# Kernel tuning notes

Measured on AMD Instinct MI355X. Metric: run time of the kernel, lower is better.

The kernel has to match this reference:

```python
import math
import jax, jax.numpy as jnp
import numpy as np

B, T = 2, 2048
D_MODEL, D_HEAD = 2048, 128
N_Q, N_KV = 16, 4
QPG = N_Q // N_KV  # queries per kv group
ROPE_BASE = 10000.0
YARN_SCALE = 4.0
ORIG_MAX_LEN = 4096
BETA_FAST, BETA_SLOW = 32.0, 1.0
RMS_EPS = 1.1920929e-07  # torch.finfo(float32).eps (nn.RMSNorm default)


def _yarn_inv_freq():
    inv = 1.0 / ROPE_BASE ** (np.arange(0, D_HEAD, 2, dtype=np.float32) / D_HEAD)
    wavelengths = 2.0 * math.pi / inv
    low_wavelen = ORIG_MAX_LEN / BETA_SLOW
    high_wavelen = ORIG_MAX_LEN / BETA_FAST
    gamma = np.clip((low_wavelen - wavelengths) / (low_wavelen - high_wavelen), 0.0, 1.0)
    return (gamma * inv + (1.0 - gamma) * inv / YARN_SCALE).astype(np.float32)

INV_FREQ = jnp.asarray(_yarn_inv_freq())  # (D_HEAD//2,) constant buffer
MSCALE = 0.1 * math.log(YARN_SCALE) + 1.0
ATTN_SCALE = 1.0 / (MSCALE * math.sqrt(D_HEAD))


def _rms_norm(x, w):
    # normalize over last dim (d_head), learnable per-dim weight
    return x * jax.lax.rsqrt(jnp.mean(x * x, axis=-1, keepdims=True) + RMS_EPS) * w


def _apply_rope(x):
    # x: (..., T, d_head)
    t = jnp.arange(x.shape[-2], dtype=jnp.float32)
    freqs = jnp.outer(t, INV_FREQ)                 # (T, d/2)
    emb = jnp.concatenate([freqs, freqs], axis=-1)  # (T, d)
    cos, sin = jnp.cos(emb), jnp.sin(emb)
    half = x.shape[-1] // 2
    x_rot = jnp.concatenate([-x[..., half:], x[..., :half]], axis=-1)
    return x * cos + x_rot * sin


def setup_inputs() -> dict:
    key = jax.random.key(0)
    ks = jax.random.split(key, 5)
    x = jax.random.normal(ks[0], (B, T, D_MODEL), dtype=jnp.float32)
    w_scale = 0.02
    Wq = jax.random.normal(ks[1], (D_MODEL, N_Q * D_HEAD), dtype=jnp.float32) * w_scale
    Wkv = jax.random.normal(ks[2], (D_MODEL, 2 * N_KV * D_HEAD), dtype=jnp.float32) * w_scale
    Wo = jax.random.normal(ks[3], (N_Q * D_HEAD, D_MODEL), dtype=jnp.float32) * w_scale
    q_norm_w = jnp.ones((D_HEAD,), dtype=jnp.float32)
    k_norm_w = jnp.ones((D_HEAD,), dtype=jnp.float32)
    return {"x": x, "Wq": Wq, "Wkv": Wkv, "Wo": Wo,
            "q_norm_w": q_norm_w, "k_norm_w": k_norm_w}


def reference(x, Wq, Wkv, Wo, q_norm_w, k_norm_w):
    b, t, _ = x.shape
    # projections
    q = (x @ Wq).reshape(b, t, QPG, N_KV, D_HEAD).transpose(0, 2, 3, 1, 4)  # (b,qpg,g,t,d)
    kv = x @ Wkv
    k, v = jnp.split(kv, 2, axis=-1)
    k = k.reshape(b, t, N_KV, D_HEAD).transpose(0, 2, 1, 3)  # (b,g,t,d)
    v = v.reshape(b, t, N_KV, D_HEAD).transpose(0, 2, 1, 3)  # (b,g,t,d)
    # RMSNorm + YaRN RoPE on q,k (math done in float32 as in source)
    q = _apply_rope(_rms_norm(q, q_norm_w))
    k = _apply_rope(_rms_norm(k, k_norm_w))
    # GQA replication: head index h = qpg*N_KV + g (matches source rearrange/reshape)
    q = q.reshape(b, N_Q, t, D_HEAD)
    k = jnp.broadcast_to(k[:, None], (b, QPG, N_KV, t, D_HEAD)).reshape(b, N_Q, t, D_HEAD)
    v = jnp.broadcast_to(v[:, None], (b, QPG, N_KV, t, D_HEAD)).reshape(b, N_Q, t, D_HEAD)
    # causal SDPA with custom scale
    scores = jnp.einsum('bhtd,bhsd->bhts', q, k) * ATTN_SCALE
    causal = jnp.tril(jnp.ones((t, t), dtype=bool))
    scores = jnp.where(causal, scores, jnp.finfo(scores.dtype).min)
    probs = jax.nn.softmax(scores, axis=-1)
    attn = jnp.einsum('bhts,bhsd->bhtd', probs, v)
    out = attn.transpose(0, 2, 1, 3).reshape(b, t, N_Q * D_HEAD)
    return out @ Wo
```

## Files before the change

kernel.cpp:

```cpp
#include <hip/hip_runtime.h>
#include <cmath>

typedef float f32x4 __attribute__((ext_vector_type(4)));
typedef __bf16 bf16x8 __attribute__((ext_vector_type(8)));

#define DEV static __device__ __forceinline__

DEV unsigned short f2bf(float f) {
  unsigned int u = __builtin_bit_cast(unsigned int, f);
  u += 0x7FFFu + ((u >> 16) & 1u);
  return (unsigned short)(u >> 16);
}
DEV float bf2f(unsigned short h) {
  unsigned int u = ((unsigned int)h) << 16;
  return __builtin_bit_cast(float, u);
}
DEV unsigned int cvtpk(float lo, float hi) {
  unsigned int r;
  asm("v_cvt_pk_bf16_f32 %0, %1, %2" : "=v"(r) : "v"(lo), "v"(hi));
  return r;
}
DEV f32x4 mfma16(bf16x8 a, bf16x8 b, f32x4 c) {
  return __builtin_amdgcn_mfma_f32_16x16x32_bf16(a, b, c, 0, 0, 0);
}
DEV void dma16(const void* g, void* l) {
  __builtin_amdgcn_global_load_lds(
      (const __attribute__((address_space(1))) void*)(uintptr_t)g,
      (__attribute__((address_space(3))) void*)(unsigned int)(uintptr_t)l,
      16, 0, 0);
}

constexpr int T_SEQ = 2048;

__global__ __launch_bounds__(256) void build_rope(float2* __restrict__ rope) {
  int gid = blockIdx.x * 256 + threadIdx.x;
  if (gid >= T_SEQ * 64) return;
  int t = gid >> 6, i = gid & 63;
  double inv = pow(10000.0, -((double)(2 * i)) / 128.0);
  double wl = 6.283185307179586 / inv;
  double gm = (4096.0 - wl) / (4096.0 - 128.0);
  gm = gm < 0.0 ? 0.0 : (gm > 1.0 ? 1.0 : gm);
  float f = (float)(gm * inv + (1.0 - gm) * inv * 0.25);
  float th = (float)t * f;
  float s, c;
  sincosf(th, &s, &c);
  rope[gid] = make_float2(c, s);
}

__global__ __launch_bounds__(256) void cvt_f32_bf16(const float4* __restrict__ in,
                                                    ushort* __restrict__ out, int n4) {
  int i = blockIdx.x * 256 + threadIdx.x;
  if (i >= n4) return;
  float4 v = in[i];
  unsigned int lo = (unsigned int)f2bf(v.x) | ((unsigned int)f2bf(v.y) << 16);
  unsigned int hi = (unsigned int)f2bf(v.z) | ((unsigned int)f2bf(v.w) << 16);
  int row = i >> 9;
  int e = (i * 4) & 2047;
  size_t o = ((size_t)row << 11) + (size_t)(e ^ ((row & 7) << 3));
  *(uint2*)(out + o) = make_uint2(lo, hi);
}

__global__ __launch_bounds__(256) void tconv(const float* __restrict__ in,
                                             ushort* __restrict__ out, int R, int C) {
  __shared__ ushort tile[64][65];
  int c0 = blockIdx.x * 64, r0 = blockIdx.y * 64;
  int j = threadIdx.x & 63, i0 = threadIdx.x >> 6;
#pragma unroll
  for (int ii = 0; ii < 16; ++ii) {
    int i = i0 + ii * 4;
    tile[i][j] = f2bf(in[(size_t)(r0 + i) * C + c0 + j]);
  }
  __syncthreads();
#pragma unroll
  for (int ii = 0; ii < 16; ++ii) {
    int jr = i0 + ii * 4;
    out[(size_t)(c0 + jr) * R + ((r0 + j) ^ ((jr & 7) << 3))] = tile[j][jr];
  }
}

template <int BM, int OUT_BF16>
__global__ __launch_bounds__(512) void gemm256(const ushort* __restrict__ A,
                                               const ushort* __restrict__ Bt,
                                               void* __restrict__ Cv,
                                               int M, int N, int K) {
  constexpr int MT = BM / 32;
  constexpr int NPH = MT / 2;
  constexpr int ADMA = BM / 64;
  __shared__ ushort lA[2][BM * 64];
  __shared__ ushort lB[2][256 * 64];
  const int tid = threadIdx.x, lane = tid & 63, w = tid >> 6;
  const int wm = (w >> 2) * (BM / 2);
  const int wn = (w & 3) * 64;
  const int m0 = blockIdx.y * BM, n0 = blockIdx.x * 256;

  f32x4 acc[MT][4] = {};

  const size_t K2 = (size_t)K * 2;
  const char* Ab = (const char*)A + (size_t)m0 * K2;
  const char* Bb = (const char*)Bt + (size_t)n0 * K2;
  const int srb = lane >> 3;
  const int scb = (lane & 7) * 16;

  auto stage = [&](int t, int bi) {
#pragma unroll
    for (int ii = 0; ii < ADMA; ++ii) {
      const int ar = w * (BM / 8) + ii * 8;
      dma16(Ab + (size_t)(ar + srb) * K2 + (size_t)t * 128 + scb,
            (char*)lA[bi] + ar * 128);
    }
#pragma unroll
    for (int ii = 0; ii < 4; ++ii) {
      const int br = w * 32 + ii * 8;
      dma16(Bb + (size_t)(br + srb) * K2 + (size_t)t * 128 + scb,
            (char*)lB[bi] + br * 128);
    }
  };

  stage(0, 0);
  const int nkt = K >> 6;

  for (int t = 0; t < nkt; ++t) {
    const int cur = t & 1;
    if (t + 1 < nkt) {
      stage(t + 1, cur ^ 1);
      if constexpr (BM == 256)
        asm volatile("s_waitcnt vmcnt(8)" ::: "memory");
      else
        asm volatile("s_waitcnt vmcnt(6)" ::: "memory");
    } else {
      asm volatile("s_waitcnt vmcnt(0)" ::: "memory");
    }
    __builtin_amdgcn_s_barrier();
    __builtin_amdgcn_sched_barrier(0);

    const char* lAc = (const char*)lA[cur];
    const char* lBc = (const char*)lB[cur];

#pragma unroll
    for (int ph = 0; ph < NPH; ++ph) {
      const int mb = (BM == 256) ? (ph >> 1) * 4 : 0;
      const int nb = (BM == 256) ? (ph & 1) * 2 : ph * 2;
#pragma unroll
      for (int kk = 0; kk < 2; ++kk) {
        bf16x8 af[4], bfr[2];
        const int byo = kk * 64 + ((lane >> 4) << 4);
#pragma unroll
        for (int i = 0; i < 4; ++i) {
          int row = wm + (mb + i) * 16 + (lane & 15);
          af[i] = *(const bf16x8*)(lAc + row * 128 + (byo ^ ((row & 7) << 4)));
        }
#pragma unroll
        for (int i = 0; i < 2; ++i) {
          int row = wn + (nb + i) * 16 + (lane & 15);
          bfr[i] = *(const bf16x8*)(lBc + row * 128 + (byo ^ ((row & 7) << 4)));
        }
        __builtin_amdgcn_s_setprio(1);
#pragma unroll
        for (int i = 0; i < 4; ++i)
#pragma unroll
          for (int j = 0; j < 2; ++j)
            acc[mb + i][nb + j] = mfma16(af[i], bfr[j], acc[mb + i][nb + j]);
        __builtin_amdgcn_s_setprio(0);
      }
    }
    __builtin_amdgcn_sched_barrier(0);
    __builtin_amdgcn_s_barrier();
  }

  const int rr = (lane >> 4) << 2;
  const int cc = lane & 15;
  if (OUT_BF16) {
    ushort* C = (ushort*)Cv;
#pragma unroll
    for (int mt = 0; mt < MT; ++mt)
#pragma unroll
      for (int nt = 0; nt < 4; ++nt)
#pragma unroll
        for (int j = 0; j < 4; ++j) {
          int r = m0 + wm + mt * 16 + rr + j;
          int c = n0 + wn + nt * 16 + cc;
          C[(size_t)r * N + c] = f2bf(acc[mt][nt][j]);
        }
  } else {
    float* C = (float*)Cv;
#pragma unroll
    for (int mt = 0; mt < MT; ++mt)
#pragma unroll
      for (int nt = 0; nt < 4; ++nt)
#pragma unroll
        for (int j = 0; j < 4; ++j) {
          int r = m0 + wm + mt * 16 + rr + j;
          int c = n0 + wn + nt * 16 + cc;
          C[(size_t)r * N + c] = acc[mt][nt][j];
        }
  }
}

__global__ __launch_bounds__(256) void norm_rope(const ushort* __restrict__ qkv,
                                                 const float* __restrict__ qw,
                                                 const float* __restrict__ kw,
                                                 const float2* __restrict__ rope,
                                                 ushort* __restrict__ qout,
                                                 ushort* __restrict__ kout,
                                                 float q_scale) {
  const int w = threadIdx.x >> 6, lane = threadIdx.x & 63;
  const int vi = blockIdx.x * 4 + w;
  const ushort* src;
  const float* wt;
  ushort* dst;
  float extra;
  int t, bb;
  if (vi < 65536) {
    int row = vi >> 4, H = vi & 15;
    bb = row >> 11;
    t = row & 2047;
    src = qkv + (size_t)row * 3072 + H * 128 + lane * 2;
    wt = qw;
    extra = q_scale;
    dst = qout + ((size_t)(bb * 16 + H) * T_SEQ + t) * 128 + lane * 2;
  } else {
    int vi2 = vi - 65536;
    int row = vi2 >> 2, gg = vi2 & 3;
    bb = row >> 11;
    t = row & 2047;
    src = qkv + (size_t)row * 3072 + 2048 + gg * 128 + lane * 2;
    wt = kw;
    extra = 1.f;
    dst = kout + ((size_t)(bb * 4 + gg) * T_SEQ + t) * 128 +
          ((lane * 2) ^ ((t & 7) << 3));
  }
  float x0 = bf2f(src[0]), x1 = bf2f(src[1]);
  float ss = x0 * x0 + x1 * x1;
#pragma unroll
  for (int d = 1; d < 64; d <<= 1) ss += __shfl_xor(ss, d, 64);
  float sc = rsqrtf(ss * (1.f / 128.f) + 1.1920929e-7f);
  float w0 = wt[lane * 2], w1 = wt[lane * 2 + 1];
  float xn0 = x0 * sc * w0, xn1 = x1 * sc * w1;
  float p0 = __shfl_xor(xn0, 32, 64), p1 = __shfl_xor(xn1, 32, 64);
  float r0 = lane < 32 ? -p0 : p0;
  float r1 = lane < 32 ? -p1 : p1;
  int i0 = (lane * 2) & 63;
  float2 cs0 = rope[t * 64 + i0];
  float2 cs1 = rope[t * 64 + i0 + 1];
  float o0 = (xn0 * cs0.x + r0 * cs0.y) * extra;
  float o1 = (xn1 * cs1.x + r1 * cs1.y) * extra;
  unsigned int pk = (unsigned int)f2bf(o0) | ((unsigned int)f2bf(o1) << 16);
  *(unsigned int*)dst = pk;
}

__global__ __launch_bounds__(256) void tv_kernel(const ushort* __restrict__ qkv,
                                                 ushort* __restrict__ vt) {
  __shared__ ushort tile[64][65];
  int t0 = blockIdx.x * 64;
  int y = blockIdx.y;
  int dh = y & 1, bg = y >> 1;
  int bb = bg >> 2, g = bg & 3;
  int j = threadIdx.x & 63, i0 = threadIdx.x >> 6;
#pragma unroll
  for (int ii = 0; ii < 16; ++ii) {
    int i = i0 + ii * 4;
    tile[i][j] = qkv[(size_t)(bb * T_SEQ + t0 + i) * 3072 + 2560 + g * 128 + dh * 64 + j];
  }
  __syncthreads();
#pragma unroll
  for (int ii = 0; ii < 16; ++ii) {
    int jr = i0 + ii * 4;
    vt[((size_t)bg * 128 + dh * 64 + jr) * T_SEQ + ((t0 + j) ^ ((jr & 7) << 3))] = tile[j][jr];
  }
}

__global__ __launch_bounds__(256, 2) void attn_fwd(const ushort* __restrict__ qh,
                                                   const ushort* __restrict__ kh,
                                                   const ushort* __restrict__ vt,
                                                   ushort* __restrict__ o) {
  const int f = blockIdx.x;
  const int half = f >> 8, c = f & 255;
  const int kk = c >> 5, bh = c & 31;
  const int qt = half ? kk : (15 - kk);
  const int b = bh >> 4, H = bh & 15;
  const int g = H & 3;
  const int tid = threadIdx.x, lane = tid & 63, w = tid >> 6;
  const int wrow0 = qt * 128 + w * 32;

  __shared__ ushort lK[2][64 * 128];
  __shared__ ushort lV[2][128 * 64];
  __shared__ ushort lP[4 * 32 * 64];

  bf16x8 qf[2][4];
#pragma unroll
  for (int mt = 0; mt < 2; ++mt) {
    const ushort* qb = qh + ((size_t)(b * 16 + H) * T_SEQ + wrow0 + mt * 16 + (lane & 15)) * 128 +
                       ((lane >> 4) << 3);
#pragma unroll
    for (int kc = 0; kc < 4; ++kc) qf[mt][kc] = *(const bf16x8*)(qb + kc * 32);
  }

  f32x4 oacc[2][8] = {};
  float mrow[2] = {-INFINITY, -INFINITY};
  float lrow[2] = {0.f, 0.f};

  const char* kpl = (const char*)(kh + (size_t)(b * 4 + g) * T_SEQ * 128);
  const char* vpl = (const char*)(vt + (size_t)(b * 4 + g) * 128 * T_SEQ);

  auto stage = [&](int j, int bi) {
#pragma unroll
    for (int ii = 0; ii < 4; ++ii) {
      const int off = w * 4096 + ii * 1024;
      dma16(kpl + (size_t)j * 16384 + off + lane * 16, (char*)lK[bi] + off);
      const int vrow = w * 32 + ii * 8 + (lane >> 3);
      dma16(vpl + (size_t)vrow * (T_SEQ * 2) + j * 128 + (lane & 7) * 16,
            (char*)lV[bi] + off);
    }
  };

  stage(0, 0);

  const int rsel = ((lane >> 4) << 2);

  const int jmax = 2 * qt + 1;
  for (int j = 0; j <= jmax; ++j) {
    const int cur = j & 1;
    if (j < jmax) {
      stage(j + 1, cur ^ 1);
      asm volatile("s_waitcnt vmcnt(8)" ::: "memory");
    } else {
      asm volatile("s_waitcnt vmcnt(0)" ::: "memory");
    }
    __builtin_amdgcn_s_barrier();
    __builtin_amdgcn_sched_barrier(0);

    f32x4 s[2][4];
#pragma unroll
    for (int nt = 0; nt < 4; ++nt) {
      bf16x8 kf[4];
      int krow = nt * 16 + (lane & 15);
#pragma unroll
      for (int kc = 0; kc < 4; ++kc) {
        int byo = kc * 64 + ((lane >> 4) << 4);
        kf[kc] = *(const bf16x8*)((const char*)lK[cur] + krow * 256 + (byo ^ ((krow & 7) << 4)));
      }
#pragma unroll
      for (int mt = 0; mt < 2; ++mt) {
        f32x4 a = {0.f, 0.f, 0.f, 0.f};
#pragma unroll
        for (int kc = 0; kc < 4; ++kc) a = mfma16(kf[kc], qf[mt][kc], a);
        s[mt][nt] = a;
      }
    }

    if (j * 64 + 63 > wrow0) {
#pragma unroll
      for (int mt = 0; mt < 2; ++mt) {
        int qrow = wrow0 + mt * 16 + (lane & 15);
#pragma unroll
        for (int nt = 0; nt < 4; ++nt)
#pragma unroll
          for (int jj = 0; jj < 4; ++jj) {
            int col = j * 64 + nt * 16 + rsel + jj;
            if (col > qrow) s[mt][nt][jj] = -3.0e38f;
          }
      }
    }

    float pm[2], mn[2];
#pragma unroll
    for (int mt = 0; mt < 2; ++mt) {
      float a0 = fmaxf(fmaxf(s[mt][0][0], s[mt][0][1]), fmaxf(s[mt][0][2], s[mt][0][3]));
      float a1 = fmaxf(fmaxf(s[mt][1][0], s[mt][1][1]), fmaxf(s[mt][1][2], s[mt][1][3]));
      float a2 = fmaxf(fmaxf(s[mt][2][0], s[mt][2][1]), fmaxf(s[mt][2][2], s[mt][2][3]));
      float a3 = fmaxf(fmaxf(s[mt][3][0], s[mt][3][1]), fmaxf(s[mt][3][2], s[mt][3][3]));
      float p = fmaxf(fmaxf(a0, a1), fmaxf(a2, a3));
      p = fmaxf(p, __shfl_xor(p, 16, 64));
      p = fmaxf(p, __shfl_xor(p, 32, 64));
      pm[mt] = p;
      mn[mt] = mrow[mt];
    }

    bool ok = (pm[0] <= mrow[0] + 11.5417f) && (pm[1] <= mrow[1] + 11.5417f);
    if (!__all(ok)) {
#pragma unroll
      for (int mt = 0; mt < 2; ++mt) {
        mn[mt] = fmaxf(mrow[mt], pm[mt]);
        float rsc = exp2f(mrow[mt] - mn[mt]);
        mrow[mt] = mn[mt];
        lrow[mt] *= rsc;
        float rr0 = __shfl(rsc, rsel + 0, 64);
        float rr1 = __shfl(rsc, rsel + 1, 64);
        float rr2 = __shfl(rsc, rsel + 2, 64);
        float rr3 = __shfl(rsc, rsel + 3, 64);
#pragma unroll
        for (int dt = 0; dt < 8; ++dt) {
          oacc[mt][dt][0] *= rr0; oacc[mt][dt][1] *= rr1;
          oacc[mt][dt][2] *= rr2; oacc[mt][dt][3] *= rr3;
        }
      }
    }

#pragma unroll
    for (int mt = 0; mt < 2; ++mt) {
      float ps = 0.f;
      int prow = mt * 16 + (lane & 15);
      char* pbase = (char*)lP + w * 4096 + prow * 128;
      int swz = (prow & 7) << 4;
#pragma unroll
      for (int nt = 0; nt < 4; ++nt) {
        float p0 = exp2f(s[mt][nt][0] - mn[mt]);
        float p1 = exp2f(s[mt][nt][1] - mn[mt]);
        float p2 = exp2f(s[mt][nt][2] - mn[mt]);
        float p3 = exp2f(s[mt][nt][3] - mn[mt]);
        ps += (p0 + p1) + (p2 + p3);
        int pcb = (nt * 32 + ((lane >> 4) << 3)) ^ swz;
        *(uint2*)(pbase + pcb) = make_uint2(cvtpk(p0, p1), cvtpk(p2, p3));
      }
      ps += __shfl_xor(ps, 16, 64);
      ps += __shfl_xor(ps, 32, 64);
      lrow[mt] += ps;
    }

#pragma unroll
    for (int kc2 = 0; kc2 < 2; ++kc2) {
      bf16x8 pa[2];
#pragma unroll
      for (int mt = 0; mt < 2; ++mt) {
        int prow = mt * 16 + (lane & 15);
        int pbo = kc2 * 64 + ((lane >> 4) << 4);
        pa[mt] = *(const bf16x8*)((char*)lP + w * 4096 + prow * 128 + (pbo ^ ((prow & 7) << 4)));
      }
#pragma unroll
      for (int dt = 0; dt < 8; ++dt) {
        int vrow = dt * 16 + (lane & 15);
        int vbo = kc2 * 64 + ((lane >> 4) << 4);
        bf16x8 vf = *(const bf16x8*)((const char*)lV[cur] + vrow * 128 + (vbo ^ ((vrow & 7) << 4)));
#pragma unroll
        for (int mt = 0; mt < 2; ++mt) oacc[mt][dt] = mfma16(pa[mt], vf, oacc[mt][dt]);
      }
    }

    __builtin_amdgcn_sched_barrier(0);
    __builtin_amdgcn_s_barrier();
  }

#pragma unroll
  for (int mt = 0; mt < 2; ++mt) {
    float linv = 1.f / lrow[mt];
    float iv0 = __shfl(linv, rsel + 0, 64);
    float iv1 = __shfl(linv, rsel + 1, 64);
    float iv2 = __shfl(linv, rsel + 2, 64);
    float iv3 = __shfl(linv, rsel + 3, 64);
    int row = wrow0 + mt * 16 + rsel;
#pragma unroll
    for (int dt = 0; dt < 8; ++dt) {
      int col = H * 128 + dt * 16 + (lane & 15);
      o[(size_t)(b * T_SEQ + row + 0) * 2048 + (col ^ (((row + 0) & 7) << 3))] =
          f2bf(oacc[mt][dt][0] * iv0);
      o[(size_t)(b * T_SEQ + row + 1) * 2048 + (col ^ (((row + 1) & 7) << 3))] =
          f2bf(oacc[mt][dt][1] * iv1);
      o[(size_t)(b * T_SEQ + row + 2) * 2048 + (col ^ (((row + 2) & 7) << 3))] =
          f2bf(oacc[mt][dt][2] * iv2);
      o[(size_t)(b * T_SEQ + row + 3) * 2048 + (col ^ (((row + 3) & 7) << 3))] =
          f2bf(oacc[mt][dt][3] * iv3);
    }
  }
}

extern "C" void kernel_launch(void* const* d_in, const int* in_sizes, int n_in,
                              void* d_out, int out_size, void* d_ws, size_t ws_size,
                              hipStream_t stream) {
  (void)in_sizes; (void)n_in; (void)out_size; (void)ws_size;
  const float* x = (const float*)d_in[0];
  const float* Wq = (const float*)d_in[1];
  const float* Wkv = (const float*)d_in[2];
  const float* Wo = (const float*)d_in[3];
  const float* qnw = (const float*)d_in[4];
  const float* knw = (const float*)d_in[5];
  float* out = (float*)d_out;
  char* ws = (char*)d_ws;

  ushort* xb = (ushort*)(ws);
  ushort* wqkv = (ushort*)(ws + 16777216);
  ushort* wot = (ushort*)(ws + 29360128);
  ushort* qkvraw = (ushort*)(ws + 37748736);
  ushort* kh = (ushort*)(ws + 62914560);
  ushort* vtp = (ushort*)(ws + 67108864);
  float2* rope = (float2*)(ws + 71303168);
  ushort* qh = xb;
  ushort* attnb = qkvraw;

  float attn_scale = 1.0f / ((0.1f * logf(4.0f) + 1.0f) * sqrtf(128.0f));
  float q_scale = attn_scale * 1.44269504f;

  build_rope<<<512, 256, 0, stream>>>(rope);
  cvt_f32_bf16<<<8192, 256, 0, stream>>>((const float4*)x, xb, 2097152);
  tconv<<<dim3(32, 32), 256, 0, stream>>>(Wq, wqkv, 2048, 2048);
  tconv<<<dim3(16, 32), 256, 0, stream>>>(Wkv, wqkv + (size_t)2048 * 2048, 2048, 1024);
  tconv<<<dim3(32, 32), 256, 0, stream>>>(Wo, wot, 2048, 2048);
  gemm256<256, 1><<<dim3(12, 16), 512, 0, stream>>>(xb, wqkv, qkvraw, 4096, 3072, 2048);
  norm_rope<<<20480, 256, 0, stream>>>(qkvraw, qnw, knw, rope, qh, kh, q_scale);
  tv_kernel<<<dim3(32, 16), 256, 0, stream>>>(qkvraw, vtp);
  attn_fwd<<<512, 256, 0, stream>>>(qh, kh, vtp, attnb);
  gemm256<128, 0><<<dim3(8, 32), 512, 0, stream>>>(attnb, wot, out, 4096, 2048, 2048);
}
```

Measured before the change: 221.2 us.

## Pre-pack GEMM operands into tile-contiguous MFMA fragment layout

Introduces a packed layout in which each 64-wide K tile of a row panel is stored contiguously in the order the MFMA fragments are read. The conversion, transpose and attention-output kernels now write this layout, so the GEMM can DMA contiguous 1 KB chunks and read LDS fragments with simple strided offsets instead of swizzled row addressing. This aims to cut global-load address scatter and LDS address arithmetic in both GEMMs. In exchange the producer kernels do scattered writes, and the attention epilogue's per-element stores get more complex index math.

Result: slower. 233.3 us (+5.5%).

```diff
diff --git a/kernel.cpp b/kernel.cpp
--- a/kernel.cpp
+++ b/kernel.cpp
@@ -28,6 +28,15 @@
       (const __attribute__((address_space(1))) void*)(uintptr_t)g,
       (__attribute__((address_space(3))) void*)(unsigned int)(uintptr_t)l,
       16, 0, 0);
+}
+
+DEV size_t pk(int row, int col, int TR) {
+  int pm = row / TR;
+  int rl = row & (TR - 1);
+  int t = col >> 6;
+  int kc = col & 63;
+  int s = ((rl >> 4) << 7) + ((kc >> 5) << 6) + (rl & 15) + (((kc >> 3) & 3) << 4);
+  return ((size_t)(pm * 32 + t) * (TR * 8) + s) * 8 + (kc & 7);
 }
 
 constexpr int T_SEQ = 2048;
@@ -48,20 +57,23 @@
 }
 
 __global__ __launch_bounds__(256) void cvt_f32_bf16(const float4* __restrict__ in,
-                                                    ushort* __restrict__ out, int n4) {
+                                                    ushort* __restrict__ out, int n8) {
   int i = blockIdx.x * 256 + threadIdx.x;
-  if (i >= n4) return;
-  float4 v = in[i];
-  unsigned int lo = (unsigned int)f2bf(v.x) | ((unsigned int)f2bf(v.y) << 16);
-  unsigned int hi = (unsigned int)f2bf(v.z) | ((unsigned int)f2bf(v.w) << 16);
-  int row = i >> 9;
-  int e = (i * 4) & 2047;
-  size_t o = ((size_t)row << 11) + (size_t)(e ^ ((row & 7) << 3));
-  *(uint2*)(out + o) = make_uint2(lo, hi);
+  if (i >= n8) return;
+  float4 v0 = in[i * 2], v1 = in[i * 2 + 1];
+  int row = i >> 8;
+  int col = (i & 255) * 8;
+  uint4 o;
+  o.x = (unsigned int)f2bf(v0.x) | ((unsigned int)f2bf(v0.y) << 16);
+  o.y = (unsigned int)f2bf(v0.z) | ((unsigned int)f2bf(v0.w) << 16);
+  o.z = (unsigned int)f2bf(v1.x) | ((unsigned int)f2bf(v1.y) << 16);
+  o.w = (unsigned int)f2bf(v1.z) | ((unsigned int)f2bf(v1.w) << 16);
+  *(uint4*)(out + pk(row, col, 256)) = o;
 }
 
 __global__ __launch_bounds__(256) void tconv(const float* __restrict__ in,
-                                             ushort* __restrict__ out, int R, int C) {
+                                             ushort* __restrict__ out, int R, int C,
+                                             int nbase) {
   __shared__ ushort tile[64][65];
   int c0 = blockIdx.x * 64, r0 = blockIdx.y * 64;
   int j = threadIdx.x & 63, i0 = threadIdx.x >> 6;
@@ -74,45 +86,40 @@
 #pragma unroll
   for (int ii = 0; ii < 16; ++ii) {
     int jr = i0 + ii * 4;
-    out[(size_t)(c0 + jr) * R + ((r0 + j) ^ ((jr & 7) << 3))] = tile[j][jr];
-  }
-}
-
-template <int BM, int OUT_BF16>
-__global__ __launch_bounds__(512) void gemm256(const ushort* __restrict__ A,
-                                               const ushort* __restrict__ Bt,
+    out[pk(nbase + c0 + jr, r0 + j, 256)] = tile[j][jr];
+  }
+}
+
+template <int TRA, int OUT_BF16>
+__global__ __launch_bounds__(512) void gemm256(const ushort* __restrict__ Apk,
+                                               const ushort* __restrict__ Bpk,
                                                void* __restrict__ Cv,
-                                               int M, int N, int K) {
-  constexpr int MT = BM / 32;
+                                               int N, int K) {
+  constexpr int MT = TRA / 32;
   constexpr int NPH = MT / 2;
-  constexpr int ADMA = BM / 64;
-  __shared__ ushort lA[2][BM * 64];
+  constexpr int ADMA = TRA / 64;
+  __shared__ ushort lA[2][TRA * 64];
   __shared__ ushort lB[2][256 * 64];
   const int tid = threadIdx.x, lane = tid & 63, w = tid >> 6;
-  const int wm = (w >> 2) * (BM / 2);
+  const int wm = (w >> 2) * (TRA / 2);
   const int wn = (w & 3) * 64;
-  const int m0 = blockIdx.y * BM, n0 = blockIdx.x * 256;
+  const int pm = blockIdx.y, pn = blockIdx.x;
+  const int m0 = pm * TRA, n0 = pn * 256;
 
   f32x4 acc[MT][4] = {};
 
-  const size_t K2 = (size_t)K * 2;
-  const char* Ab = (const char*)A + (size_t)m0 * K2;
-  const char* Bb = (const char*)Bt + (size_t)n0 * K2;
-  const int srb = lane >> 3;
-  const int scb = (lane & 7) * 16;
-
   auto stage = [&](int t, int bi) {
 #pragma unroll
     for (int ii = 0; ii < ADMA; ++ii) {
-      const int ar = w * (BM / 8) + ii * 8;
-      dma16(Ab + (size_t)(ar + srb) * K2 + (size_t)t * 128 + scb,
-            (char*)lA[bi] + ar * 128);
+      const int L = w * ADMA + ii;
+      dma16((const char*)Apk + ((size_t)(pm * 32 + t) * (TRA * 8) + L * 64 + lane) * 16,
+            (char*)lA[bi] + L * 1024);
     }
 #pragma unroll
     for (int ii = 0; ii < 4; ++ii) {
-      const int br = w * 32 + ii * 8;
-      dma16(Bb + (size_t)(br + srb) * K2 + (size_t)t * 128 + scb,
-            (char*)lB[bi] + br * 128);
+      const int L = w * 4 + ii;
+      dma16((const char*)Bpk + ((size_t)(pn * 32 + t) * 2048 + L * 64 + lane) * 16,
+            (char*)lB[bi] + L * 1024);
     }
   };
 
@@ -123,7 +130,7 @@
     const int cur = t & 1;
     if (t + 1 < nkt) {
       stage(t + 1, cur ^ 1);
-      if constexpr (BM == 256)
+      if constexpr (TRA == 256)
         asm volatile("s_waitcnt vmcnt(8)" ::: "memory");
       else
         asm volatile("s_waitcnt vmcnt(6)" ::: "memory");
@@ -133,33 +140,28 @@
     __builtin_amdgcn_s_barrier();
     __builtin_amdgcn_sched_barrier(0);
 
-    const char* lAc = (const char*)lA[cur];
-    const char* lBc = (const char*)lB[cur];
+    const char* lAc = (const char*)lA[cur] + (size_t)(wm >> 4) * 2048 + lane * 16;
+    const char* lBc = (const char*)lB[cur] + (size_t)(wn >> 4) * 2048 + lane * 16;
 
 #pragma unroll
     for (int ph = 0; ph < NPH; ++ph) {
-      const int mb = (BM == 256) ? (ph >> 1) * 4 : 0;
-      const int nb = (BM == 256) ? (ph & 1) * 2 : ph * 2;
+      const int mb = (TRA == 256) ? (ph >> 1) * 4 : 0;
+      const int nb = (TRA == 256) ? (ph & 1) * 2 : ph * 2;
 #pragma unroll
       for (int kk = 0; kk < 2; ++kk) {
         bf16x8 af[4], bfr[2];
-        const int byo = kk * 64 + ((lane >> 4) << 4);
-#pragma unroll
-        for (int i = 0; i < 4; ++i) {
-          int row = wm + (mb + i) * 16 + (lane & 15);
-          af[i] = *(const bf16x8*)(lAc + row * 128 + (byo ^ ((row & 7) << 4)));
-        }
-#pragma unroll
-        for (int i = 0; i < 2; ++i) {
-          int row = wn + (nb + i) * 16 + (lane & 15);
-          bfr[i] = *(const bf16x8*)(lBc + row * 128 + (byo ^ ((row & 7) << 4)));
-        }
+#pragma unroll
+        for (int i = 0; i < 4; ++i)
+          af[i] = *(const bf16x8*)(lAc + ((mb + i) * 2 + kk) * 1024);
+#pragma unroll
+        for (int i = 0; i < 2; ++i)
+          bfr[i] = *(const bf16x8*)(lBc + ((nb + i) * 2 + kk) * 1024);
         __builtin_amdgcn_s_setprio(1);
 #pragma unroll
         for (int i = 0; i < 4; ++i)
 #pragma unroll
-          for (int j = 0; j < 2; ++j)
-            acc[mb + i][nb + j] = mfma16(af[i], bfr[j], acc[mb + i][nb + j]);
+          for (int jj = 0; jj < 2; ++jj)
+            acc[mb + i][nb + jj] = mfma16(af[i], bfr[jj], acc[mb + i][nb + jj]);
         __builtin_amdgcn_s_setprio(0);
       }
     }
@@ -244,8 +246,8 @@
   float2 cs1 = rope[t * 64 + i0 + 1];
   float o0 = (xn0 * cs0.x + r0 * cs0.y) * extra;
   float o1 = (xn1 * cs1.x + r1 * cs1.y) * extra;
-  unsigned int pk = (unsigned int)f2bf(o0) | ((unsigned int)f2bf(o1) << 16);
-  *(unsigned int*)dst = pk;
+  unsigned int pkv = (unsigned int)f2bf(o0) | ((unsigned int)f2bf(o1) << 16);
+  *(unsigned int*)dst = pkv;
 }
 
 __global__ __launch_bounds__(256) void tv_kernel(const ushort* __restrict__ qkv,
@@ -362,7 +364,7 @@
       }
     }
 
-    float pm[2], mn[2];
+    float pmx[2], mn[2];
 #pragma unroll
     for (int mt = 0; mt < 2; ++mt) {
       float a0 = fmaxf(fmaxf(s[mt][0][0], s[mt][0][1]), fmaxf(s[mt][0][2], s[mt][0][3]));
@@ -372,15 +374,15 @@
       float p = fmaxf(fmaxf(a0, a1), fmaxf(a2, a3));
       p = fmaxf(p, __shfl_xor(p, 16, 64));
       p = fmaxf(p, __shfl_xor(p, 32, 64));
-      pm[mt] = p;
+      pmx[mt] = p;
       mn[mt] = mrow[mt];
     }
 
-    bool ok = (pm[0] <= mrow[0] + 11.5417f) && (pm[1] <= mrow[1] + 11.5417f);
+    bool ok = (pmx[0] <= mrow[0] + 11.5417f) && (pmx[1] <= mrow[1] + 11.5417f);
     if (!__all(ok)) {
 #pragma unroll
       for (int mt = 0; mt < 2; ++mt) {
-        mn[mt] = fmaxf(mrow[mt], pm[mt]);
+        mn[mt] = fmaxf(mrow[mt], pmx[mt]);
         float rsc = exp2f(mrow[mt] - mn[mt]);
         mrow[mt] = mn[mt];
         lrow[mt] *= rsc;
@@ -447,18 +449,14 @@
     float iv1 = __shfl(linv, rsel + 1, 64);
     float iv2 = __shfl(linv, rsel + 2, 64);
     float iv3 = __shfl(linv, rsel + 3, 64);
-    int row = wrow0 + mt * 16 + rsel;
+    int row = b * T_SEQ + wrow0 + mt * 16 + rsel;
 #pragma unroll
     for (int dt = 0; dt < 8; ++dt) {
       int col = H * 128 + dt * 16 + (lane & 15);
-      o[(size_t)(b * T_SEQ + row + 0) * 2048 + (col ^ (((row + 0) & 7) << 3))] =
-          f2bf(oacc[mt][dt][0] * iv0);
-      o[(size_t)(b * T_SEQ + row + 1) * 2048 + (col ^ (((row + 1) & 7) << 3))] =
-          f2bf(oacc[mt][dt][1] * iv1);
-      o[(size_t)(b * T_SEQ + row + 2) * 2048 + (col ^ (((row + 2) & 7) << 3))] =
-          f2bf(oacc[mt][dt][2] * iv2);
-      o[(size_t)(b * T_SEQ + row + 3) * 2048 + (col ^ (((row + 3) & 7) << 3))] =
-          f2bf(oacc[mt][dt][3] * iv3);
+      o[pk(row + 0, col, 128)] = f2bf(oacc[mt][dt][0] * iv0);
+      o[pk(row + 1, col, 128)] = f2bf(oacc[mt][dt][1] * iv1);
+      o[pk(row + 2, col, 128)] = f2bf(oacc[mt][dt][2] * iv2);
+      o[pk(row + 3, col, 128)] = f2bf(oacc[mt][dt][3] * iv3);
     }
   }
 }
@@ -490,13 +488,13 @@
   float q_scale = attn_scale * 1.44269504f;
 
   build_rope<<<512, 256, 0, stream>>>(rope);
-  cvt_f32_bf16<<<8192, 256, 0, stream>>>((const float4*)x, xb, 2097152);
-  tconv<<<dim3(32, 32), 256, 0, stream>>>(Wq, wqkv, 2048, 2048);
-  tconv<<<dim3(16, 32), 256, 0, stream>>>(Wkv, wqkv + (size_t)2048 * 2048, 2048, 1024);
-  tconv<<<dim3(32, 32), 256, 0, stream>>>(Wo, wot, 2048, 2048);
-  gemm256<256, 1><<<dim3(12, 16), 512, 0, stream>>>(xb, wqkv, qkvraw, 4096, 3072, 2048);
+  cvt_f32_bf16<<<4096, 256, 0, stream>>>((const float4*)x, xb, 1048576);
+  tconv<<<dim3(32, 32), 256, 0, stream>>>(Wq, wqkv, 2048, 2048, 0);
+  tconv<<<dim3(16, 32), 256, 0, stream>>>(Wkv, wqkv, 2048, 1024, 2048);
+  tconv<<<dim3(32, 32), 256, 0, stream>>>(Wo, wot, 2048, 2048, 0);
+  gemm256<256, 1><<<dim3(12, 16), 512, 0, stream>>>(xb, wqkv, qkvraw, 3072, 2048);
   norm_rope<<<20480, 256, 0, stream>>>(qkvraw, qnw, knw, rope, qh, kh, q_scale);
   tv_kernel<<<dim3(32, 16), 256, 0, stream>>>(qkvraw, vtp);
   attn_fwd<<<512, 256, 0, stream>>>(qh, kh, vtp, attnb);
-  gemm256<128, 0><<<dim3(8, 32), 512, 0, stream>>>(attnb, wot, out, 4096, 2048, 2048);
-}
+  gemm256<128, 0><<<dim3(8, 32), 512, 0, stream>>>(attnb, wot, out, 2048, 2048);
+}
```
